# Optimization experiments

Measured on AMD Instinct MI355X. Metric: run time of the kernel, lower is better.

The kernel has to match this reference:

```python
import jax, jax.numpy as jnp
import numpy as np

NS, NV, NB, L = 64, 32, 8, 4      # scalar channels, vector channels, bessel bases, layers
EMB = 32                           # atom-type embedding dim
MAX_R = 3.0                        # cutoff radius
NUM_NEIGH = 32.0                   # avg degree used for scatter normalization
N, E = 10000, 320000
NW = NS * 2 + NV * 2               # per-edge tensor-product weights from radial MLP
MAX_TYPES = 10


def smooth_cutoff(x):
    # e3nn md-example smooth_cutoff: 1 for x<0.5, 0 for x>1, cosine blend between
    u = 2.0 * (x - 1.0)
    y = (1.0 - jnp.cos(jnp.pi * u)) * 0.5
    y = jnp.where(u > 0.0, 0.0, y)
    y = jnp.where(u < -1.0, 1.0, y)
    return y


def bessel_basis(r):
    # soft_one_hot_linspace(basis='bessel', cutoff=False) * sqrt(NB)
    n = jnp.arange(1, NB + 1, dtype=r.dtype)
    y = jnp.sqrt(2.0 / MAX_R) * jnp.sin(n * jnp.pi * r[:, None] / MAX_R) / r[:, None]
    return y * np.sqrt(NB).astype(np.float32)


def edge_info(x, src, dst):
    feats, attrs = [], []
    for i in range(2):  # nvec = x.shape[-1] // 3 = 2
        vec = x[src, 3 * i:3 * i + 3] - x[dst, 3 * i:3 * i + 3]  # [E,3]
        r = jnp.linalg.norm(vec, axis=1)
        sh = np.float32(np.sqrt(3.0)) * vec / r[:, None]          # 1x1o SH, component norm
        feats.append(bessel_basis(r))
        attrs.append(smooth_cutoff(r / MAX_R)[:, None] * sh)
    return jnp.concatenate(feats, axis=-1), jnp.stack(attrs, axis=1)  # [E,2*NB], [E,2,3]


def _forward(x, emb_table, W_up, W_proj, fc1, b1, fc2, W_sv, W_vs, W_sc_s, W_sc_v, Ws, Wv, h, mix, node_attr, edge_src, edge_dst):
    n = x.shape[0]
    inv_nb = np.float32(1.0 / np.sqrt(NUM_NEIGH))
    # uplift: 2 input vectors -> NV hidden vectors, NS hidden scalars (zero init)
    xv = x.reshape(n, 2, 3)
    v = jnp.einsum('nic,iv->nvc', xv, W_up)        # [n,NV,3]
    s = jnp.zeros((n, NS), x.dtype)                # [n,NS]
    s_old, v_old = s, v
    attr_emb = emb_table[node_attr]                # [n,EMB]
    xcur = x
    for i in range(L):
        f, a = edge_info(xcur, edge_src, edge_dst)            # [E,2NB], [E,2,3]
        w = jax.nn.silu(f @ fc1[i] + b1[i]) @ fc2[i]          # [E,NW] radial TP weights
        w1 = w[:, :NS * 2].reshape(-1, NS, 2)                 # 0e x 1o -> 1o path weights
        w2 = w[:, NS * 2:].reshape(-1, NV, 2)                 # 1o x 1o -> 0e path weights
        # equivariant tensor-product messages (gather at edge_src)
        t = s[edge_src][:, :, None] * w1                      # [E,NS,2]
        q = jnp.einsum('euv,uvm->evm', t, W_sv[i])            # [E,2,NV]
        msg_v = jnp.einsum('evm,evc->emc', q, a)              # [E,NV,3]
        d = jnp.einsum('euc,evc->euv', v[edge_src], a)        # [E,NV,2]
        msg_s = jnp.einsum('euv,uvm->em', d * w2, W_vs[i])    # [E,NS+NV]
        # scatter-add at edge_dst, normalized by sqrt(num_neighbors)
        agg_s = jnp.zeros((n, NS + NV), x.dtype).at[edge_dst].add(msg_s) * inv_nb
        agg_v = jnp.zeros((n, NV, 3), x.dtype).at[edge_dst].add(msg_v) * inv_nb
        # self-connection: fully-connected TP with node-attr scalars
        sc_s = jnp.einsum('nu,ne,uem->nm', s, attr_emb, W_sc_s[i])
        sc_v = jnp.einsum('nuc,ne,uev->nvc', v, attr_emb, W_sc_v[i])
        cs = sc_s + agg_s
        cv = sc_v + agg_v
        # Gate: silu on scalars, sigmoid gate scalars modulate vectors
        gs = jax.nn.silu(cs[:, :NS])
        gate = jax.nn.sigmoid(cs[:, NS:])
        gv = cv * gate[:, :, None]
        # self-interaction (equivariant linear per degree)
        si_s = s @ Ws[i]
        si_v = jnp.einsum('nuc,uv->nvc', v, Wv[i])
        # verlet-like update
        hi2 = h[i] ** 2
        s_new = 2.0 * s - s_old + hi2 * (mix[i] * gs + (mix[i] - 1.0) * si_s)
        v_new = 2.0 * v - v_old + hi2 * (mix[i] * gv + (mix[i] - 1.0) * si_v)
        s_old, v_old = s, v
        s, v = s_new, v_new
        # project back to x for next layer's edge features
        xcur = jnp.einsum('nvc,vi->nic', v, W_proj).reshape(n, 6)
    return xcur


def setup_inputs() -> dict:
    key = jax.random.key(0)
    ks = jax.random.split(key, 20)
    x = jax.random.normal(ks[0], (N, 6), jnp.float32)
    node_attr = jax.random.randint(ks[1], (N,), 0, MAX_TYPES)
    edge_src = jax.random.randint(ks[2], (E,), 0, N)
    off = jax.random.randint(ks[3], (E,), 1, N)
    edge_dst = (edge_src + off) % N  # no self-loops -> no zero edge_vec
    batch = jnp.zeros((N,), jnp.int32)
    rn = lambda k, sh, sc: jax.random.normal(k, sh, jnp.float32) * np.float32(sc)
    emb_table = rn(ks[4], (MAX_TYPES, EMB), 0.5)
    W_up = rn(ks[5], (2, NV), 1.0 / np.sqrt(2))
    W_proj = rn(ks[6], (NV, 2), 1.0 / np.sqrt(NV))
    fc1 = rn(ks[7], (L, 2 * NB, 64), 1.0 / np.sqrt(2 * NB))
    b1 = jnp.zeros((L, 64), jnp.float32)
    fc2 = rn(ks[8], (L, 64, NW), 1.0 / np.sqrt(64))
    W_sv = rn(ks[9], (L, NS, 2, NV), 1.0 / np.sqrt(NS * 2))
    W_vs = rn(ks[10], (L, NV, 2, NS + NV), 1.0 / np.sqrt(NV * 2))
    W_sc_s = rn(ks[11], (L, NS, EMB, NS + NV), 1.0 / np.sqrt(NS * EMB))
    W_sc_v = rn(ks[12], (L, NV, EMB, NV), 1.0 / np.sqrt(NV * EMB))
    Ws = rn(ks[13], (L, NS, NS), 1.0 / np.sqrt(NS))
    Wv = rn(ks[14], (L, NV, NV), 1.0 / np.sqrt(NV))
    h = jnp.ones((L,), jnp.float32) * 0.01
    mix = jnp.ones((L,), jnp.float32) * 0.5
    return {"x": x, "emb_table": emb_table, "W_up": W_up, "W_proj": W_proj, "fc1": fc1, "b1": b1, "fc2": fc2, "W_sv": W_sv, "W_vs": W_vs, "W_sc_s": W_sc_s, "W_sc_v": W_sc_v, "Ws": Ws, "Wv": Wv, "h": h, "mix": mix, "node_attr": node_attr, "edge_src": edge_src, "edge_dst": edge_dst, "batch": batch}


def reference(x, emb_table, W_up, W_proj, fc1, b1, fc2, W_sv, W_vs, W_sc_s, W_sc_v, Ws, Wv, h, mix, node_attr, edge_src, edge_dst, batch):
    return _forward(x, emb_table, W_up, W_proj, fc1, b1, fc2, W_sv, W_vs, W_sc_s, W_sc_v, Ws, Wv, h, mix, node_attr, edge_src, edge_dst)
```

## Files before the change

### kernel.cpp

```cpp
#include <hip/hip_runtime.h>
#include <math.h>

constexpr int cNS = 64, cNV = 32, cNB = 8, cL = 4, cEMB = 32, cNT = 10;
constexpr float PI_F = 3.14159265358979323846f;
constexpr float INV_SQRT_NN = 0.17677669529663687f;
constexpr float BESSEL_C = 2.3094010767585034f;
constexpr float SQRT3 = 1.7320508075688772f;

typedef unsigned short u16;
typedef unsigned int u32;
typedef __attribute__((ext_vector_type(8))) short bf16x8;
typedef __attribute__((ext_vector_type(4))) float f32x4;
typedef __attribute__((ext_vector_type(2))) float f32x2;
typedef __attribute__((ext_vector_type(4))) int i32x4;

__device__ __forceinline__ u16 f2b(float x) {
  u32 u = __float_as_uint(x);
  return (u16)((u + 0x7fffu + ((u >> 16) & 1u)) >> 16);
}
__device__ __forceinline__ float b2f(u16 h) { return __uint_as_float(((u32)h) << 16); }
__device__ __forceinline__ float blo(u32 w) { return __uint_as_float(w << 16); }
__device__ __forceinline__ float bhi(u32 w) { return __uint_as_float(w & 0xffff0000u); }

__device__ __forceinline__ u32 pkbf(float lo, float hi) {
  u32 r;
  asm("v_cvt_pk_bf16_f32 %0, %1, %2" : "=v"(r) : "v"(lo), "v"(hi));
  return r;
}

union U8 { bf16x8 v; u32 w[4]; };

__device__ __forceinline__ f32x4 mfma16(bf16x8 a, bf16x8 b, f32x4 c) {
  return __builtin_amdgcn_mfma_f32_16x16x32_bf16(a, b, c, 0, 0, 0);
}


__global__ void k_precompA(const float* __restrict__ emb, const float* __restrict__ Wss,
                           float* __restrict__ A) {
  int idx = blockIdx.x * 256 + threadIdx.x;
  if (idx >= cL * cNT * 64 * 96) return;
  int m = idx % 96;
  int u = (idx / 96) % 64;
  int t = (idx / (96 * 64)) % cNT;
  int l = idx / (96 * 64 * cNT);
  float acc = 0.f;
#pragma unroll
  for (int e = 0; e < 32; ++e)
    acc += emb[t * 32 + e] * Wss[((size_t)(l * 64 + u) * 32 + e) * 96 + m];
  A[idx] = acc;
}

__global__ void k_precompB(const float* __restrict__ emb, const float* __restrict__ Wsv_,
                           float* __restrict__ B) {
  int idx = blockIdx.x * 256 + threadIdx.x;
  if (idx >= cL * cNT * 32 * 32) return;
  int vo = idx % 32;
  int u = (idx / 32) % 32;
  int t = (idx / 1024) % cNT;
  int l = idx / (1024 * cNT);
  float acc = 0.f;
#pragma unroll
  for (int e = 0; e < 32; ++e)
    acc += emb[t * 32 + e] * Wsv_[((size_t)(l * 32 + u) * 32 + e) * 32 + vo];
  B[idx] = acc;
}

__global__ void k_packB(const float* __restrict__ fc2, const float* __restrict__ Wsv,
                        const float* __restrict__ Wvs, const float* __restrict__ fc1,
                        u16* __restrict__ fc2L, u16* __restrict__ WsvL,
                        u16* __restrict__ WvsL, u16* __restrict__ fc1L) {
  int idx = blockIdx.x * 256 + threadIdx.x;
  const int T1 = cL * 12288, T2 = cL * 2 * 2048, T3 = cL * 2 * 3072, T4 = cL * 2048;
  if (idx < T1) {
    int l = idx / 12288, r = idx % 12288;
    int ki = r & 7, tt = r >> 3;
    int nn = tt % 192, kq = tt / 192;
    fc2L[idx] = f2b(fc2[((size_t)(l * 64) + kq * 8 + ki) * 192 + nn]);
  } else if (idx < T1 + T2) {
    int r0 = idx - T1;
    int l = r0 / 4096, r1 = r0 % 4096;
    int k2 = r1 / 2048, r = r1 % 2048;
    int ki = r & 7, tt = r >> 3;
    int mm = tt % 32, kq = tt / 32;
    WsvL[r0] = f2b(Wsv[((size_t)((l * 64 + kq * 8 + ki) * 2) + k2) * 32 + mm]);
  } else if (idx < T1 + T2 + T3) {
    int r0 = idx - T1 - T2;
    int l = r0 / 6144, r1 = r0 % 6144;
    int k2 = r1 / 3072, r = r1 % 3072;
    int ki = r & 7, tt = r >> 3;
    int mm = tt % 96, kq = tt / 96;
    WvsL[r0] = f2b(Wvs[((size_t)((l * 32 + kq * 8 + ki) * 2) + k2) * 96 + mm]);
  } else if (idx < T1 + T2 + T3 + T4) {
    int r0 = idx - T1 - T2 - T3;
    int l = r0 / 2048, r1 = r0 % 2048;
    int kq = r1 / 512, rem = r1 % 512;
    int n = rem / 8, ki = rem & 7;
    fc1L[r0] = (kq < 2) ? f2b(fc1[l * 1024 + (kq * 8 + ki) * 64 + n]) : (u16)0;
  }
}

__global__ void k_init(const float* __restrict__ x, const float* __restrict__ Wup,
                       float* __restrict__ v, float* __restrict__ v_old,
                       float* __restrict__ xcur, int N) {
  int idx = blockIdx.x * 256 + threadIdx.x;
  if (idx >= N * 32) return;
  int n = idx >> 5, vc = idx & 31;
  float w0 = Wup[vc], w1 = Wup[32 + vc];
#pragma unroll
  for (int c = 0; c < 3; ++c) {
    float val = x[n * 6 + c] * w0 + x[n * 6 + 3 + c] * w1;
    v[idx * 3 + c] = val;
    v_old[idx * 3 + c] = val;
  }
  if (vc < 6) xcur[n * 6 + vc] = x[n * 6 + vc];
}


__global__ void k_zero_i(int* __restrict__ p, int n) {
  int i = blockIdx.x * 256 + threadIdx.x;
  if (i < n) p[i] = 0;
}

__global__ void k_hist(const int* __restrict__ edst, int* __restrict__ deg, int E) {
  int e = blockIdx.x * 256 + threadIdx.x;
  if (e < E) atomicAdd(&deg[edst[e]], 1);
}

__global__ __launch_bounds__(1024) void k_scan(const int* __restrict__ deg,
                                               int* __restrict__ row_ptr,
                                               int* __restrict__ cursor, int N) {
  __shared__ int part[1024];
  int t = threadIdx.x;
  int chunk = (N + 1023) / 1024;
  int base = t * chunk;
  int sum = 0;
  for (int i = 0; i < chunk; ++i) {
    int idx = base + i;
    if (idx < N) sum += deg[idx];
  }
  part[t] = sum;
  __syncthreads();
  for (int off = 1; off < 1024; off <<= 1) {
    int val = (t >= off) ? part[t - off] : 0;
    __syncthreads();
    part[t] += val;
    __syncthreads();
  }
  int run = (t > 0) ? part[t - 1] : 0;
  for (int i = 0; i < chunk; ++i) {
    int idx = base + i;
    if (idx < N) {
      row_ptr[idx] = run;
      cursor[idx] = run;
      run += deg[idx];
    }
  }
  if (t == 1023) row_ptr[N] = part[1023];
}

__global__ void k_scatter(const int* __restrict__ esrc, const int* __restrict__ edst,
                          int* __restrict__ cursor, int* __restrict__ esrc_s,
                          int* __restrict__ edst_s, int E) {
  int e = blockIdx.x * 256 + threadIdx.x;
  if (e < E) {
    int d = edst[e];
    int p = atomicAdd(&cursor[d], 1);
    esrc_s[p] = esrc[e];
    edst_s[p] = d;
  }
}

template <bool SZERO>
__global__ __launch_bounds__(256) void k_edge_mfma(
    const float* __restrict__ xcur, const float* __restrict__ s, const float* __restrict__ v,
    const int* __restrict__ esrc_s, const int* __restrict__ edst_s,
    const u16* __restrict__ fc1L, const float* __restrict__ b1,
    const u16* __restrict__ fc2L, const u16* __restrict__ WsvL0,
    const u16* __restrict__ WsvL1, const u16* __restrict__ WvsL0,
    const u16* __restrict__ WvsL1, u16* __restrict__ msgbuf, int E) {
  __shared__ u16 wbAll[4][16 * 200];
  __shared__ float aAll[4][16][6];
  int wid = threadIdx.x >> 6, lane = threadIdx.x & 63;
  int e0 = (blockIdx.x * 4 + wid) * 16;
  if (e0 >= E) return;
  u16* wb = wbAll[wid];
  int lrow = lane & 15, lg = lane >> 4;

  {
    int el = lane >> 2, qq = lane & 3;
    int ge = e0 + el;
    if (ge >= E) ge = E - 1;
    int gs = esrc_s[ge], gd = edst_s[ge];
    float xs[6], xd[6];
    {
      const float2* ps = (const float2*)(xcur + (size_t)gs * 6);
      const float2* pd = (const float2*)(xcur + (size_t)gd * 6);
      float2 A0 = ps[0], A1 = ps[1], A2 = ps[2];
      float2 B0 = pd[0], B1 = pd[1], B2 = pd[2];
      xs[0] = A0.x; xs[1] = A0.y; xs[2] = A1.x; xs[3] = A1.y; xs[4] = A2.x; xs[5] = A2.y;
      xd[0] = B0.x; xd[1] = B0.y; xd[2] = B1.x; xd[3] = B1.y; xd[4] = B2.x; xd[5] = B2.y;
    }
    float f[16], av[6];
#pragma unroll
    for (int i = 0; i < 2; ++i) {
      float vx = xs[3 * i + 0] - xd[3 * i + 0];
      float vy = xs[3 * i + 1] - xd[3 * i + 1];
      float vz = xs[3 * i + 2] - xd[3 * i + 2];
      float r2 = vx * vx + vy * vy + vz * vz;
      float rr = sqrtf(r2);
      float invr = 1.0f / rr;
      float th = (PI_F / 3.0f) * rr;
      float s1, c1;
      __sincosf(th, &s1, &c1);
      float twc = 2.0f * c1;
      float snm = 0.f, sn = s1;
      float fc = BESSEL_C * invr;
#pragma unroll
      for (int nn = 0; nn < 8; ++nn) {
        f[8 * i + nn] = fc * sn;
        float nx = twc * sn - snm;
        snm = sn;
        sn = nx;
      }
      float uu = (2.0f / 3.0f) * rr - 2.0f;
      float cut;
      if (uu > 0.f) cut = 0.f;
      else if (uu < -1.f) cut = 1.f;
      else cut = (1.0f - __cosf(PI_F * uu)) * 0.5f;
      float sc = cut * SQRT3 * invr;
      av[3 * i + 0] = vx * sc; av[3 * i + 1] = vy * sc; av[3 * i + 2] = vz * sc;
    }
    if (qq == 0) {
      u32* fp = (u32*)(wb + 1600 + el * 32);
#pragma unroll
      for (int i = 0; i < 8; ++i) fp[i] = pkbf(f[2 * i], f[2 * i + 1]);
#pragma unroll
      for (int i = 8; i < 16; ++i) fp[i] = 0u;
      float* ap = aAll[wid][el];
#pragma unroll
      for (int i = 0; i < 6; ++i) ap[i] = av[i];
    }
  }
  asm volatile("s_waitcnt lgkmcnt(0)" ::: "memory");
  __builtin_amdgcn_sched_barrier(0);

  {
    bf16x8 fA = *(const bf16x8*)(wb + 1600 + lrow * 32 + lg * 8);
    f32x4 hp[4];
#pragma unroll
    for (int nb = 0; nb < 4; ++nb) {
      bf16x8 bB = *(const bf16x8*)(fc1L + (size_t)(lg * 64 + nb * 16 + lrow) * 8);
      f32x4 z = {0.f, 0.f, 0.f, 0.f};
      hp[nb] = mfma16(fA, bB, z);
    }
#pragma unroll
    for (int nb = 0; nb < 4; ++nb) {
      float bias = b1[nb * 16 + lrow];
      float hv[4];
#pragma unroll
      for (int r = 0; r < 4; ++r) {
        float xv = hp[nb][r] + bias;
        hv[r] = xv * (1.0f / (1.0f + __expf(-xv)));
      }
      u32 p01 = pkbf(hv[0], hv[1]);
      u32 p23 = pkbf(hv[2], hv[3]);
      int col = nb * 16 + lrow;
      wb[(4 * lg + 0) * 72 + col] = (u16)p01;
      wb[(4 * lg + 1) * 72 + col] = (u16)(p01 >> 16);
      wb[(4 * lg + 2) * 72 + col] = (u16)p23;
      wb[(4 * lg + 3) * 72 + col] = (u16)(p23 >> 16);
    }
  }
  asm volatile("s_waitcnt lgkmcnt(0)" ::: "memory");
  __builtin_amdgcn_sched_barrier(0);

  int prow = e0 + lrow;
  if (prow >= E) prow = E - 1;

  bf16x8 ha = *(const bf16x8*)(wb + lrow * 72 + lg * 8);
  bf16x8 hbf = *(const bf16x8*)(wb + lrow * 72 + 32 + lg * 8);
  asm volatile("s_waitcnt lgkmcnt(0)" ::: "memory");

#pragma unroll
  for (int nb = (SZERO ? 8 : 0); nb < 12; ++nb) {
    bf16x8 b0 = *(const bf16x8*)(fc2L + (size_t)(lg * 192 + nb * 16 + lrow) * 8);
    bf16x8 b1v = *(const bf16x8*)(fc2L + (size_t)((4 + lg) * 192 + nb * 16 + lrow) * 8);
    f32x4 c = {0.f, 0.f, 0.f, 0.f};
    c = mfma16(ha, b0, c);
    c = mfma16(hbf, b1v, c);
    int n = nb * 16 + lrow;
    int pn = (n < 128) ? ((n & 1) * 64 + (n >> 1)) : (128 + (n & 1) * 32 + ((n - 128) >> 1));
    int rbase = 4 * lg * 200 + pn;
    u32 p01 = pkbf(c[0], c[1]);
    u32 p23 = pkbf(c[2], c[3]);
    wb[rbase] = (u16)p01;
    wb[rbase + 200] = (u16)(p01 >> 16);
    wb[rbase + 400] = (u16)p23;
    wb[rbase + 600] = (u16)(p23 >> 16);
  }
  asm volatile("s_waitcnt lgkmcnt(0)" ::: "memory");

  int src = esrc_s[prow];
  const u16* wrow = wb + lrow * 200;

  f32x4 q0[2], q1[2];
  if (!SZERO) {
    const float* sp = s + (size_t)src * 64;
    float sv0[8], sv1[8];
    *(f32x4*)(sv0) = *(const f32x4*)(sp + lg * 8);
    *(f32x4*)(sv0 + 4) = *(const f32x4*)(sp + lg * 8 + 4);
    *(f32x4*)(sv1) = *(const f32x4*)(sp + 32 + lg * 8);
    *(f32x4*)(sv1 + 4) = *(const f32x4*)(sp + 32 + lg * 8 + 4);
    i32x4 W0a = *(const i32x4*)(wrow + lg * 8);
    i32x4 W0b = *(const i32x4*)(wrow + 32 + lg * 8);
    i32x4 W1a = *(const i32x4*)(wrow + 64 + lg * 8);
    i32x4 W1b = *(const i32x4*)(wrow + 96 + lg * 8);
    U8 t0a, t0b, t1a, t1b;
#pragma unroll
    for (int j2 = 0; j2 < 4; ++j2) {
      u32 wa = (u32)W0a[j2], wbv = (u32)W0b[j2], wc = (u32)W1a[j2], wd = (u32)W1b[j2];
      t0a.w[j2] = pkbf(sv0[2 * j2] * blo(wa), sv0[2 * j2 + 1] * bhi(wa));
      t0b.w[j2] = pkbf(sv1[2 * j2] * blo(wbv), sv1[2 * j2 + 1] * bhi(wbv));
      t1a.w[j2] = pkbf(sv0[2 * j2] * blo(wc), sv0[2 * j2 + 1] * bhi(wc));
      t1b.w[j2] = pkbf(sv1[2 * j2] * blo(wd), sv1[2 * j2 + 1] * bhi(wd));
    }
#pragma unroll
    for (int nb = 0; nb < 2; ++nb) {
      bf16x8 bA = *(const bf16x8*)(WsvL0 + (size_t)(lg * 32 + nb * 16 + lrow) * 8);
      bf16x8 bB = *(const bf16x8*)(WsvL0 + (size_t)((4 + lg) * 32 + nb * 16 + lrow) * 8);
      f32x4 c = {0.f, 0.f, 0.f, 0.f};
      c = mfma16(t0a.v, bA, c);
      c = mfma16(t0b.v, bB, c);
      q0[nb] = c;
      bf16x8 bC = *(const bf16x8*)(WsvL1 + (size_t)(lg * 32 + nb * 16 + lrow) * 8);
      bf16x8 bD = *(const bf16x8*)(WsvL1 + (size_t)((4 + lg) * 32 + nb * 16 + lrow) * 8);
      f32x4 c2 = {0.f, 0.f, 0.f, 0.f};
      c2 = mfma16(t1a.v, bC, c2);
      c2 = mfma16(t1b.v, bD, c2);
      q1[nb] = c2;
    }
  }

  float a00, a01, a02, a10, a11, a12;
  {
    const float* ap = aAll[wid][lrow];
    a00 = ap[0]; a01 = ap[1]; a02 = ap[2]; a10 = ap[3]; a11 = ap[4]; a12 = ap[5];
  }
  float vl[24];
  {
    const float* vp = v + (size_t)src * 96 + lg * 24;
#pragma unroll
    for (int i = 0; i < 6; ++i) *(f32x4*)(vl + 4 * i) = *(const f32x4*)(vp + 4 * i);
  }
  i32x4 W2a = *(const i32x4*)(wrow + 128 + lg * 8);
  i32x4 W2b = *(const i32x4*)(wrow + 160 + lg * 8);
  U8 ga, gb;
#pragma unroll
  for (int j2 = 0; j2 < 4; ++j2) {
    float d0a, d1a, d0b, d1b;
    {
      float vx = vl[6 * j2 + 0], vy = vl[6 * j2 + 1], vz = vl[6 * j2 + 2];
      d0a = vx * a00 + vy * a01 + vz * a02;
      d1a = vx * a10 + vy * a11 + vz * a12;
    }
    {
      float vx = vl[6 * j2 + 3], vy = vl[6 * j2 + 4], vz = vl[6 * j2 + 5];
      d0b = vx * a00 + vy * a01 + vz * a02;
      d1b = vx * a10 + vy * a11 + vz * a12;
    }
    u32 wa = (u32)W2a[j2], wbv = (u32)W2b[j2];
    ga.w[j2] = pkbf(d0a * blo(wa), d0b * bhi(wa));
    gb.w[j2] = pkbf(d1a * blo(wbv), d1b * bhi(wbv));
  }
  f32x4 mS[6];
#pragma unroll
  for (int nb = 0; nb < 6; ++nb) {
    bf16x8 b0 = *(const bf16x8*)(WvsL0 + (size_t)(lg * 96 + nb * 16 + lrow) * 8);
    bf16x8 b1v = *(const bf16x8*)(WvsL1 + (size_t)(lg * 96 + nb * 16 + lrow) * 8);
    f32x4 c = {0.f, 0.f, 0.f, 0.f};
    c = mfma16(ga.v, b0, c);
    c = mfma16(gb.v, b1v, c);
    mS[nb] = c;
  }

  asm volatile("s_waitcnt lgkmcnt(0)" ::: "memory");
#pragma unroll
  for (int nb = 0; nb < 6; ++nb) {
    u32 p01 = pkbf(mS[nb][0], mS[nb][1]);
    u32 p23 = pkbf(mS[nb][2], mS[nb][3]);
    int col = nb * 16 + lrow;
    wb[(4 * lg + 0) * 200 + col] = (u16)p01;
    wb[(4 * lg + 1) * 200 + col] = (u16)(p01 >> 16);
    wb[(4 * lg + 2) * 200 + col] = (u16)p23;
    wb[(4 * lg + 3) * 200 + col] = (u16)(p23 >> 16);
  }
  if (!SZERO) {
#pragma unroll
    for (int nb = 0; nb < 2; ++nb) {
#pragma unroll
      for (int r = 0; r < 4; ++r) {
        int el = 4 * lg + r;
        const float* ap = aAll[wid][el];
        float Q0v = q0[nb][r], Q1v = q1[nb][r];
        float v0 = Q0v * ap[0] + Q1v * ap[3];
        float v1 = Q0v * ap[1] + Q1v * ap[4];
        float v2 = Q0v * ap[2] + Q1v * ap[5];
        u32 p01 = pkbf(v0, v1);
        int base = el * 200 + 96 + nb * 16 + lrow;
        wb[base] = (u16)p01;
        wb[base + 32] = (u16)(p01 >> 16);
        wb[base + 64] = f2b(v2);
      }
    }
  }
  asm volatile("s_waitcnt lgkmcnt(0)" ::: "memory");

  int orow = lane >> 2, oq = lane & 3;
  if (e0 + orow < E) {
    const int OST = SZERO ? 96 : 192;
    u16* gdst = msgbuf + (size_t)(e0 + orow) * OST;
    const int NIT = SZERO ? 3 : 6;
#pragma unroll
    for (int it = 0; it < NIT; ++it) {
      int col = oq * 8 + it * 32;
      i32x4 d = *(const i32x4*)(wb + orow * 200 + col);
      *(i32x4*)(gdst + col) = d;
    }
  }
}

template <bool SZERO>
__global__ __launch_bounds__(128) void k_gnode(
    const u16* __restrict__ msg, const int* __restrict__ row_ptr,
    float* __restrict__ s, float* __restrict__ sold, float* __restrict__ v,
    float* __restrict__ vold,
    const float* __restrict__ Amat, const float* __restrict__ Bmat,
    const float* __restrict__ Ws, const float* __restrict__ Wv,
    const float* __restrict__ Wproj, const int* __restrict__ nattr,
    const float* __restrict__ hArr, const float* __restrict__ mixArr, int layer,
    float* __restrict__ xout, int N) {
  int n = blockIdx.x;
  int t = threadIdx.x;
  __shared__ float agg[192];
  __shared__ float srow[64];
  __shared__ float vrow[96];
  __shared__ float gateS[32];
  __shared__ float vnewS[96];
  int start = row_ptr[n], end = row_ptr[n + 1];
  const int STRIDE = SZERO ? 96 : 192;
  int nacc = SZERO ? 48 : 96;
  if (t < nacc) {
    const u16* mp = msg + (size_t)t * 2;
    float aL[4] = {0.f, 0.f, 0.f, 0.f}, aH[4] = {0.f, 0.f, 0.f, 0.f};
    int p = start;
    for (; p + 8 <= end; p += 8) {
      u32 w[8];
#pragma unroll
      for (int k = 0; k < 8; ++k) w[k] = *(const u32*)(mp + (size_t)(p + k) * STRIDE);
#pragma unroll
      for (int k = 0; k < 8; ++k) {
        aL[k & 3] += blo(w[k]);
        aH[k & 3] += bhi(w[k]);
      }
    }
    for (; p < end; ++p) {
      u32 w = *(const u32*)(mp + (size_t)p * STRIDE);
      aL[0] += blo(w);
      aH[0] += bhi(w);
    }
    agg[2 * t] = (aL[0] + aL[1] + aL[2] + aL[3]) * INV_SQRT_NN;
    agg[2 * t + 1] = (aH[0] + aH[1] + aH[2] + aH[3]) * INV_SQRT_NN;
  }
  if (SZERO && t >= 48 && t < 96) {
    agg[2 * t] = 0.f;
    agg[2 * t + 1] = 0.f;
  }
  if (t < 64) srow[t] = s[(size_t)n * 64 + t];
  if (t < 96) vrow[t] = v[(size_t)n * 96 + t];
  __syncthreads();
  int type = nattr[n];
  float hv = hArr[layer];
  float h2v = hv * hv;
  float mx = mixArr[layer];
  float cs = 0.f;
  if (t < 96) {
    cs = agg[t];
    const float* Ac = Amat + (size_t)type * 64 * 96 + t;
#pragma unroll 8
    for (int u = 0; u < 64; ++u) cs += srow[u] * Ac[u * 96];
  }
  if (t >= 64 && t < 96) gateS[t - 64] = 1.0f / (1.0f + __expf(-cs));
  __syncthreads();
  if (t < 64) {
    float gs = cs * (1.0f / (1.0f + __expf(-cs)));
    float sis = 0.f;
#pragma unroll 8
    for (int u = 0; u < 64; ++u) sis += srow[u] * Ws[u * 64 + t];
    float scur = srow[t];
    float sprev = sold[(size_t)n * 64 + t];
    float snew = 2.f * scur - sprev + h2v * (mx * gs + (mx - 1.f) * sis);
    sold[(size_t)n * 64 + t] = scur;
    s[(size_t)n * 64 + t] = snew;
  }
  if (t < 96) {
    int vch = t / 3, c = t - vch * 3;
    float cv = agg[96 + c * 32 + vch];
    const float* Bc = Bmat + (size_t)type * 1024 + vch;
    float scv = 0.f, siv = 0.f;
#pragma unroll 8
    for (int u = 0; u < 32; ++u) {
      float vu = vrow[u * 3 + c];
      scv += vu * Bc[u * 32];
      siv += vu * Wv[u * 32 + vch];
    }
    cv += scv;
    float gv = cv * gateS[vch];
    float vcur = vrow[t];
    float vprev = vold[(size_t)n * 96 + t];
    float vnew = 2.f * vcur - vprev + h2v * (mx * gv + (mx - 1.f) * siv);
    vold[(size_t)n * 96 + t] = vcur;
    v[(size_t)n * 96 + t] = vnew;
    vnewS[t] = vnew;
  }
  __syncthreads();
  if (t < 6) {
    int i = t / 3, c = t - i * 3;
    float acc = 0.f;
#pragma unroll
    for (int vo = 0; vo < 32; ++vo) acc += vnewS[vo * 3 + c] * Wproj[vo * 2 + i];
    xout[(size_t)n * 6 + t] = acc;
  }
}

extern "C" void kernel_launch(void* const* d_in, const int* in_sizes, int n_in,
                              void* d_out, int out_size, void* d_ws, size_t ws_size,
                              hipStream_t stream) {
  const float* x = (const float*)d_in[0];
  const float* emb = (const float*)d_in[1];
  const float* Wup = (const float*)d_in[2];
  const float* Wproj = (const float*)d_in[3];
  const float* fc1 = (const float*)d_in[4];
  const float* b1 = (const float*)d_in[5];
  const float* fc2 = (const float*)d_in[6];
  const float* Wsv = (const float*)d_in[7];
  const float* Wvs = (const float*)d_in[8];
  const float* Wscs = (const float*)d_in[9];
  const float* Wscv = (const float*)d_in[10];
  const float* Ws = (const float*)d_in[11];
  const float* Wv = (const float*)d_in[12];
  const float* hArr = (const float*)d_in[13];
  const float* mixArr = (const float*)d_in[14];
  const int* nattr = (const int*)d_in[15];
  const int* esrc = (const int*)d_in[16];
  const int* edst = (const int*)d_in[17];

  const int N = in_sizes[0] / 6;
  const int E = in_sizes[16];

  float* ws = (float*)d_ws;
  size_t off = 0;
  auto alloc = [&](size_t nf) {
    float* p = ws + off;
    off += (nf + 3) & ~(size_t)3;
    return p;
  };
  float* sbuf = alloc((size_t)N * 64);
  float* sold = alloc((size_t)N * 64);
  float* vbuf = alloc((size_t)N * 96);
  float* vold = alloc((size_t)N * 96);
  float* xcur = alloc((size_t)N * 6);
  float* Amat = alloc((size_t)cL * cNT * 64 * 96);
  float* Bmat = alloc((size_t)cL * cNT * 32 * 32);
  u16* fc2L = (u16*)alloc((size_t)cL * 6144);
  u16* WsvL = (u16*)alloc((size_t)cL * 2048);
  u16* WvsL = (u16*)alloc((size_t)cL * 3072);
  u16* fc1L = (u16*)alloc((size_t)cL * 1024);
  int* deg = (int*)alloc((size_t)(N + 4));
  int* row_ptr = (int*)alloc((size_t)(N + 4));
  int* cursor = (int*)alloc((size_t)(N + 4));
  int* esrc_s = (int*)alloc((size_t)E);
  int* edst_s = (int*)alloc((size_t)E);
  u16* msgbuf = (u16*)alloc((size_t)E * 96);

  hipMemsetAsync(sbuf, 0, sizeof(float) * (size_t)N * 128, stream);
  k_init<<<(N * 32 + 255) / 256, 256, 0, stream>>>(x, Wup, vbuf, vold, xcur, N);
  k_precompA<<<(cL * cNT * 64 * 96 + 255) / 256, 256, 0, stream>>>(emb, Wscs, Amat);
  k_precompB<<<(cL * cNT * 32 * 32 + 255) / 256, 256, 0, stream>>>(emb, Wscv, Bmat);
  {
    int tot = cL * 12288 + cL * 4096 + cL * 6144 + cL * 2048;
    k_packB<<<(tot + 255) / 256, 256, 0, stream>>>(fc2, Wsv, Wvs, fc1, fc2L, WsvL, WvsL, fc1L);
  }
  k_zero_i<<<(N + 255) / 256, 256, 0, stream>>>(deg, N);
  k_hist<<<(E + 255) / 256, 256, 0, stream>>>(edst, deg, E);
  k_scan<<<1, 1024, 0, stream>>>(deg, row_ptr, cursor, N);
  k_scatter<<<(E + 255) / 256, 256, 0, stream>>>(esrc, edst, cursor, esrc_s, edst_s, E);

  int eblocks = ((E + 15) / 16 + 3) / 4;
  for (int l = 0; l < cL; ++l) {
    if (l == 0)
      k_edge_mfma<true><<<eblocks, 256, 0, stream>>>(
          xcur, sbuf, vbuf, esrc_s, edst_s, fc1L + l * 2048, b1 + l * 64,
          fc2L + l * 12288, WsvL + l * 4096, WsvL + l * 4096 + 2048,
          WvsL + l * 6144, WvsL + l * 6144 + 3072, msgbuf, E);
    else
      k_edge_mfma<false><<<eblocks, 256, 0, stream>>>(
          xcur, sbuf, vbuf, esrc_s, edst_s, fc1L + l * 2048, b1 + l * 64,
          fc2L + l * 12288, WsvL + l * 4096, WsvL + l * 4096 + 2048,
          WvsL + l * 6144, WvsL + l * 6144 + 3072, msgbuf, E);
    float* xout = (l == cL - 1) ? (float*)d_out : xcur;
    if (l == 0)
      k_gnode<true><<<N, 128, 0, stream>>>(
          msgbuf, row_ptr, sbuf, sold, vbuf, vold, Amat + (size_t)l * cNT * 64 * 96,
          Bmat + (size_t)l * cNT * 1024, Ws + l * 4096, Wv + l * 1024, Wproj, nattr,
          hArr, mixArr, l, xout, N);
    else
      k_gnode<false><<<N, 128, 0, stream>>>(
          msgbuf, row_ptr, sbuf, sold, vbuf, vold, Amat + (size_t)l * cNT * 64 * 96,
          Bmat + (size_t)l * cNT * 1024, Ws + l * 4096, Wv + l * 1024, Wproj, nattr,
          hArr, mixArr, l, xout, N);
  }
}
```

Measured before the change: 540.3 us.

## Swizzle edge-kernel LDS layout, hoist gathers early, and pack two nodes per block

In the edge kernel, the per-edge source-index load and the s/v feature gathers move ahead of the radial MLP so their global latency overlaps the MFMA work. The LDS layout gets an XOR swizzle on the 200-wide weight rows and a padded 40-element feature stride to cut bank conflicts. The node kernel now handles two nodes per 256-thread block with a guard on the tail node, halving block count and launch overhead. In exchange the hoisted loads raise register pressure, and the swizzle has to match on every write and read site.

```diff
diff --git a/kernel.cpp b/kernel.cpp
--- a/kernel.cpp
+++ b/kernel.cpp
@@ -33,6 +33,8 @@
 __device__ __forceinline__ f32x4 mfma16(bf16x8 a, bf16x8 b, f32x4 c) {
   return __builtin_amdgcn_mfma_f32_16x16x32_bf16(a, b, c, 0, 0, 0);
 }
+
+__device__ __forceinline__ int xm200(int row) { return ((row >> 2) & 3) << 3; }
 
 
 __global__ void k_precompA(const float* __restrict__ emb, const float* __restrict__ Wss,
@@ -186,6 +188,10 @@
   u16* wb = wbAll[wid];
   int lrow = lane & 15, lg = lane >> 4;
 
+  int prow = e0 + lrow;
+  if (prow >= E) prow = E - 1;
+  int src = esrc_s[prow];
+
   {
     int el = lane >> 2, qq = lane & 3;
     int ge = e0 + el;
@@ -231,7 +237,7 @@
       av[3 * i + 0] = vx * sc; av[3 * i + 1] = vy * sc; av[3 * i + 2] = vz * sc;
     }
     if (qq == 0) {
-      u32* fp = (u32*)(wb + 1600 + el * 32);
+      u32* fp = (u32*)(wb + 1600 + el * 40);
 #pragma unroll
       for (int i = 0; i < 8; ++i) fp[i] = pkbf(f[2 * i], f[2 * i + 1]);
 #pragma unroll
@@ -241,11 +247,26 @@
       for (int i = 0; i < 6; ++i) ap[i] = av[i];
     }
   }
+
+  float sv0[8], sv1[8], vl[24];
+  if (!SZERO) {
+    const float* sp = s + (size_t)src * 64;
+    *(f32x4*)(sv0) = *(const f32x4*)(sp + lg * 8);
+    *(f32x4*)(sv0 + 4) = *(const f32x4*)(sp + lg * 8 + 4);
+    *(f32x4*)(sv1) = *(const f32x4*)(sp + 32 + lg * 8);
+    *(f32x4*)(sv1 + 4) = *(const f32x4*)(sp + 32 + lg * 8 + 4);
+  }
+  {
+    const float* vp = v + (size_t)src * 96 + lg * 24;
+#pragma unroll
+    for (int i = 0; i < 6; ++i) *(f32x4*)(vl + 4 * i) = *(const f32x4*)(vp + 4 * i);
+  }
+
   asm volatile("s_waitcnt lgkmcnt(0)" ::: "memory");
   __builtin_amdgcn_sched_barrier(0);
 
   {
-    bf16x8 fA = *(const bf16x8*)(wb + 1600 + lrow * 32 + lg * 8);
+    bf16x8 fA = *(const bf16x8*)(wb + 1600 + lrow * 40 + lg * 8);
     f32x4 hp[4];
 #pragma unroll
     for (int nb = 0; nb < 4; ++nb) {
@@ -274,13 +295,11 @@
   asm volatile("s_waitcnt lgkmcnt(0)" ::: "memory");
   __builtin_amdgcn_sched_barrier(0);
 
-  int prow = e0 + lrow;
-  if (prow >= E) prow = E - 1;
-
   bf16x8 ha = *(const bf16x8*)(wb + lrow * 72 + lg * 8);
   bf16x8 hbf = *(const bf16x8*)(wb + lrow * 72 + 32 + lg * 8);
   asm volatile("s_waitcnt lgkmcnt(0)" ::: "memory");
 
+  int xw = lg << 3;
 #pragma unroll
   for (int nb = (SZERO ? 8 : 0); nb < 12; ++nb) {
     bf16x8 b0 = *(const bf16x8*)(fc2L + (size_t)(lg * 192 + nb * 16 + lrow) * 8);
@@ -290,7 +309,7 @@
     c = mfma16(hbf, b1v, c);
     int n = nb * 16 + lrow;
     int pn = (n < 128) ? ((n & 1) * 64 + (n >> 1)) : (128 + (n & 1) * 32 + ((n - 128) >> 1));
-    int rbase = 4 * lg * 200 + pn;
+    int rbase = 4 * lg * 200 + (pn ^ xw);
     u32 p01 = pkbf(c[0], c[1]);
     u32 p23 = pkbf(c[2], c[3]);
     wb[rbase] = (u16)p01;
@@ -300,21 +319,14 @@
   }
   asm volatile("s_waitcnt lgkmcnt(0)" ::: "memory");
 
-  int src = esrc_s[prow];
-  const u16* wrow = wb + lrow * 200;
+  const u16* wrow = wb + lrow * 200 + (((lg ^ (lrow >> 2)) & 3) << 3);
 
   f32x4 q0[2], q1[2];
   if (!SZERO) {
-    const float* sp = s + (size_t)src * 64;
-    float sv0[8], sv1[8];
-    *(f32x4*)(sv0) = *(const f32x4*)(sp + lg * 8);
-    *(f32x4*)(sv0 + 4) = *(const f32x4*)(sp + lg * 8 + 4);
-    *(f32x4*)(sv1) = *(const f32x4*)(sp + 32 + lg * 8);
-    *(f32x4*)(sv1 + 4) = *(const f32x4*)(sp + 32 + lg * 8 + 4);
-    i32x4 W0a = *(const i32x4*)(wrow + lg * 8);
-    i32x4 W0b = *(const i32x4*)(wrow + 32 + lg * 8);
-    i32x4 W1a = *(const i32x4*)(wrow + 64 + lg * 8);
-    i32x4 W1b = *(const i32x4*)(wrow + 96 + lg * 8);
+    i32x4 W0a = *(const i32x4*)(wrow);
+    i32x4 W0b = *(const i32x4*)(wrow + 32);
+    i32x4 W1a = *(const i32x4*)(wrow + 64);
+    i32x4 W1b = *(const i32x4*)(wrow + 96);
     U8 t0a, t0b, t1a, t1b;
 #pragma unroll
     for (int j2 = 0; j2 < 4; ++j2) {
@@ -346,14 +358,8 @@
     const float* ap = aAll[wid][lrow];
     a00 = ap[0]; a01 = ap[1]; a02 = ap[2]; a10 = ap[3]; a11 = ap[4]; a12 = ap[5];
   }
-  float vl[24];
-  {
-    const float* vp = v + (size_t)src * 96 + lg * 24;
-#pragma unroll
-    for (int i = 0; i < 6; ++i) *(f32x4*)(vl + 4 * i) = *(const f32x4*)(vp + 4 * i);
-  }
-  i32x4 W2a = *(const i32x4*)(wrow + 128 + lg * 8);
-  i32x4 W2b = *(const i32x4*)(wrow + 160 + lg * 8);
+  i32x4 W2a = *(const i32x4*)(wrow + 128);
+  i32x4 W2b = *(const i32x4*)(wrow + 160);
   U8 ga, gb;
 #pragma unroll
   for (int j2 = 0; j2 < 4; ++j2) {
@@ -388,11 +394,11 @@
   for (int nb = 0; nb < 6; ++nb) {
     u32 p01 = pkbf(mS[nb][0], mS[nb][1]);
     u32 p23 = pkbf(mS[nb][2], mS[nb][3]);
-    int col = nb * 16 + lrow;
-    wb[(4 * lg + 0) * 200 + col] = (u16)p01;
-    wb[(4 * lg + 1) * 200 + col] = (u16)(p01 >> 16);
-    wb[(4 * lg + 2) * 200 + col] = (u16)p23;
-    wb[(4 * lg + 3) * 200 + col] = (u16)(p23 >> 16);
+    int colx = (nb * 16 + lrow) ^ xw;
+    wb[(4 * lg + 0) * 200 + colx] = (u16)p01;
+    wb[(4 * lg + 1) * 200 + colx] = (u16)(p01 >> 16);
+    wb[(4 * lg + 2) * 200 + colx] = (u16)p23;
+    wb[(4 * lg + 3) * 200 + colx] = (u16)(p23 >> 16);
   }
   if (!SZERO) {
 #pragma unroll
@@ -406,7 +412,7 @@
         float v1 = Q0v * ap[1] + Q1v * ap[4];
         float v2 = Q0v * ap[2] + Q1v * ap[5];
         u32 p01 = pkbf(v0, v1);
-        int base = el * 200 + 96 + nb * 16 + lrow;
+        int base = el * 200 + ((96 + nb * 16 + lrow) ^ xw);
         wb[base] = (u16)p01;
         wb[base + 32] = (u16)(p01 >> 16);
         wb[base + 64] = f2b(v2);
@@ -419,18 +425,19 @@
   if (e0 + orow < E) {
     const int OST = SZERO ? 96 : 192;
     u16* gdst = msgbuf + (size_t)(e0 + orow) * OST;
+    int xo = ((orow >> 2) & 3) << 3;
     const int NIT = SZERO ? 3 : 6;
 #pragma unroll
     for (int it = 0; it < NIT; ++it) {
       int col = oq * 8 + it * 32;
-      i32x4 d = *(const i32x4*)(wb + orow * 200 + col);
+      i32x4 d = *(const i32x4*)(wb + orow * 200 + (col ^ xo));
       *(i32x4*)(gdst + col) = d;
     }
   }
 }
 
 template <bool SZERO>
-__global__ __launch_bounds__(128) void k_gnode(
+__global__ __launch_bounds__(256) void k_gnode(
     const u16* __restrict__ msg, const int* __restrict__ row_ptr,
     float* __restrict__ s, float* __restrict__ sold, float* __restrict__ v,
     float* __restrict__ vold,
@@ -439,13 +446,16 @@
     const float* __restrict__ Wproj, const int* __restrict__ nattr,
     const float* __restrict__ hArr, const float* __restrict__ mixArr, int layer,
     float* __restrict__ xout, int N) {
-  int n = blockIdx.x;
-  int t = threadIdx.x;
-  __shared__ float agg[192];
-  __shared__ float srow[64];
-  __shared__ float vrow[96];
-  __shared__ float gateS[32];
-  __shared__ float vnewS[96];
+  int half = threadIdx.x >> 7;
+  int t = threadIdx.x & 127;
+  int n = blockIdx.x * 2 + half;
+  bool active = n < N;
+  if (!active) n = N - 1;
+  __shared__ float agg[2][192];
+  __shared__ float srow[2][64];
+  __shared__ float vrow[2][96];
+  __shared__ float gateS[2][32];
+  __shared__ float vnewS[2][96];
   int start = row_ptr[n], end = row_ptr[n + 1];
   const int STRIDE = SZERO ? 96 : 192;
   int nacc = SZERO ? 48 : 96;
@@ -468,15 +478,15 @@
       aL[0] += blo(w);
       aH[0] += bhi(w);
     }
-    agg[2 * t] = (aL[0] + aL[1] + aL[2] + aL[3]) * INV_SQRT_NN;
-    agg[2 * t + 1] = (aH[0] + aH[1] + aH[2] + aH[3]) * INV_SQRT_NN;
+    agg[half][2 * t] = (aL[0] + aL[1] + aL[2] + aL[3]) * INV_SQRT_NN;
+    agg[half][2 * t + 1] = (aH[0] + aH[1] + aH[2] + aH[3]) * INV_SQRT_NN;
   }
   if (SZERO && t >= 48 && t < 96) {
-    agg[2 * t] = 0.f;
-    agg[2 * t + 1] = 0.f;
-  }
-  if (t < 64) srow[t] = s[(size_t)n * 64 + t];
-  if (t < 96) vrow[t] = v[(size_t)n * 96 + t];
+    agg[half][2 * t] = 0.f;
+    agg[half][2 * t + 1] = 0.f;
+  }
+  if (t < 64) srow[half][t] = s[(size_t)n * 64 + t];
+  if (t < 96) vrow[half][t] = v[(size_t)n * 96 + t];
   __syncthreads();
   int type = nattr[n];
   float hv = hArr[layer];
@@ -484,50 +494,54 @@
   float mx = mixArr[layer];
   float cs = 0.f;
   if (t < 96) {
-    cs = agg[t];
+    cs = agg[half][t];
     const float* Ac = Amat + (size_t)type * 64 * 96 + t;
 #pragma unroll 8
-    for (int u = 0; u < 64; ++u) cs += srow[u] * Ac[u * 96];
-  }
-  if (t >= 64 && t < 96) gateS[t - 64] = 1.0f / (1.0f + __expf(-cs));
+    for (int u = 0; u < 64; ++u) cs += srow[half][u] * Ac[u * 96];
+  }
+  if (t >= 64 && t < 96) gateS[half][t - 64] = 1.0f / (1.0f + __expf(-cs));
   __syncthreads();
   if (t < 64) {
     float gs = cs * (1.0f / (1.0f + __expf(-cs)));
     float sis = 0.f;
 #pragma unroll 8
-    for (int u = 0; u < 64; ++u) sis += srow[u] * Ws[u * 64 + t];
-    float scur = srow[t];
+    for (int u = 0; u < 64; ++u) sis += srow[half][u] * Ws[u * 64 + t];
+    float scur = srow[half][t];
     float sprev = sold[(size_t)n * 64 + t];
     float snew = 2.f * scur - sprev + h2v * (mx * gs + (mx - 1.f) * sis);
-    sold[(size_t)n * 64 + t] = scur;
-    s[(size_t)n * 64 + t] = snew;
+    if (active) {
+      sold[(size_t)n * 64 + t] = scur;
+      s[(size_t)n * 64 + t] = snew;
+    }
   }
   if (t < 96) {
     int vch = t / 3, c = t - vch * 3;
-    float cv = agg[96 + c * 32 + vch];
+    float cv = agg[half][96 + c * 32 + vch];
     const float* Bc = Bmat + (size_t)type * 1024 + vch;
     float scv = 0.f, siv = 0.f;
 #pragma unroll 8
     for (int u = 0; u < 32; ++u) {
-      float vu = vrow[u * 3 + c];
+      float vu = vrow[half][u * 3 + c];
       scv += vu * Bc[u * 32];
       siv += vu * Wv[u * 32 + vch];
     }
     cv += scv;
-    float gv = cv * gateS[vch];
-    float vcur = vrow[t];
+    float gv = cv * gateS[half][vch];
+    float vcur = vrow[half][t];
     float vprev = vold[(size_t)n * 96 + t];
     float vnew = 2.f * vcur - vprev + h2v * (mx * gv + (mx - 1.f) * siv);
-    vold[(size_t)n * 96 + t] = vcur;
-    v[(size_t)n * 96 + t] = vnew;
-    vnewS[t] = vnew;
+    if (active) {
+      vold[(size_t)n * 96 + t] = vcur;
+      v[(size_t)n * 96 + t] = vnew;
+    }
+    vnewS[half][t] = vnew;
   }
   __syncthreads();
-  if (t < 6) {
+  if (t < 6 && active) {
     int i = t / 3, c = t - i * 3;
     float acc = 0.f;
 #pragma unroll
-    for (int vo = 0; vo < 32; ++vo) acc += vnewS[vo * 3 + c] * Wproj[vo * 2 + i];
+    for (int vo = 0; vo < 32; ++vo) acc += vnewS[half][vo * 3 + c] * Wproj[vo * 2 + i];
     xout[(size_t)n * 6 + t] = acc;
   }
 }
@@ -596,6 +610,7 @@
   k_scatter<<<(E + 255) / 256, 256, 0, stream>>>(esrc, edst, cursor, esrc_s, edst_s, E);
 
   int eblocks = ((E + 15) / 16 + 3) / 4;
+  int gblocks = (N + 1) / 2;
   for (int l = 0; l < cL; ++l) {
     if (l == 0)
       k_edge_mfma<true><<<eblocks, 256, 0, stream>>>(
@@ -609,12 +624,12 @@
           WvsL + l * 6144, WvsL + l * 6144 + 3072, msgbuf, E);
     float* xout = (l == cL - 1) ? (float*)d_out : xcur;
     if (l == 0)
-      k_gnode<true><<<N, 128, 0, stream>>>(
+      k_gnode<true><<<gblocks, 256, 0, stream>>>(
           msgbuf, row_ptr, sbuf, sold, vbuf, vold, Amat + (size_t)l * cNT * 64 * 96,
           Bmat + (size_t)l * cNT * 1024, Ws + l * 4096, Wv + l * 1024, Wproj, nattr,
           hArr, mixArr, l, xout, N);
     else
-      k_gnode<false><<<N, 128, 0, stream>>>(
+      k_gnode<false><<<gblocks, 256, 0, stream>>>(
           msgbuf, row_ptr, sbuf, sold, vbuf, vold, Amat + (size_t)l * cNT * 64 * 96,
           Bmat + (size_t)l * cNT * 1024, Ws + l * 4096, Wv + l * 1024, Wproj, nattr,
           hArr, mixArr, l, xout, N);
```

Result: no change. 539.6 us (-0.1%).
